# Kernel optimization log

Measured on AMD Instinct MI355X. Metric: run time of the kernel, lower is better.

## Reference

```python
import jax, jax.numpy as jnp
import numpy as np

TEMPERATURE = 8.0  # sqrt(head_dim=64)


def sparsemax(z):
    """Sparsemax along the last axis (Martins & Astudillo 2016)."""
    S = z.shape[-1]
    z_sorted = -jnp.sort(-z, axis=-1)            # descending sort
    cs = jnp.cumsum(z_sorted, axis=-1)
    ks = jnp.arange(1, S + 1, dtype=z.dtype)
    support = 1.0 + ks * z_sorted > cs           # entries in the support set
    k_sup = jnp.sum(support, axis=-1, keepdims=True)  # support size >= 1
    tau = (jnp.take_along_axis(cs, k_sup - 1, axis=-1) - 1.0) / k_sup.astype(z.dtype)
    return jnp.maximum(z - tau, 0.0)


def setup_inputs() -> dict:
    key = jax.random.key(0)
    kq, kk, kv, km = jax.random.split(key, 4)
    B, Lq, Lk, D = 64, 1024, 1024, 64
    q = jax.random.normal(kq, (B, Lq, D), dtype=jnp.float32)
    k = jax.random.normal(kk, (B, Lk, D), dtype=jnp.float32)
    v = jax.random.normal(kv, (B, Lk, D), dtype=jnp.float32)
    mask = jax.random.randint(km, (B, Lq, Lk), 0, 2).astype(bool)  # True = masked out
    return {"q": q, "k": k, "v": v, "mask": mask}


def reference(q, k, v, mask):
    # scores: [B, Lq, Lk]
    attn = jnp.einsum('bqd,bkd->bqk', q / TEMPERATURE, k)
    # mask out disallowed keys with -inf
    attn = jnp.where(mask, -jnp.inf, attn)
    # rows where ALL keys are masked: set scores to 0 (avoids NaN in sparsemax)
    inf_mask = jnp.all(mask, axis=2, keepdims=True)  # [B, Lq, 1]
    attn = jnp.where(inf_mask, 0.0, attn)
    attn = sparsemax(attn)
    # zero out fully-masked rows again (dropout has p=0.0 -> identity in eval)
    attn = jnp.where(inf_mask, 0.0, attn)
    out = jnp.einsum('bqk,bkd->bqd', attn, v)
    return (out, attn)
```

## Files before the change

kernel.cpp:

```cpp
#include <hip/hip_runtime.h>
#include <float.h>


#define BATCH    64
#define SEQQ     1024
#define SEQK     1024
#define DHEAD    64

typedef short short8 __attribute__((ext_vector_type(8)));
typedef float f32x4  __attribute__((ext_vector_type(4)));
typedef unsigned short us4v __attribute__((ext_vector_type(4)));

typedef const __attribute__((address_space(1))) unsigned int as1_cuint;
typedef __attribute__((address_space(3))) unsigned int as3_uint;
typedef __attribute__((address_space(3))) unsigned char as3_uchar;

__device__ __forceinline__ unsigned short bf16_rne(float f) {
    unsigned u = __float_as_uint(f);
    u += 0x7fffu + ((u >> 16) & 1u);
    return (unsigned short)(u >> 16);
}

__device__ __forceinline__ void cvt_hilo8(const float* fv, float scale,
                                          short8* hi, short8* lo) {
    #pragma unroll
    for (int j = 0; j < 8; ++j) {
        float f = fv[j] * scale;
        unsigned short hb = bf16_rne(f);
        float hf = __uint_as_float((unsigned)hb << 16);
        (*hi)[j] = (short)hb;
        (*lo)[j] = (short)bf16_rne(f - hf);
    }
}

__global__ void detect_mask_fmt(const unsigned char* __restrict__ m,
                                int* __restrict__ flag) {
    __shared__ int s_found;
    if (threadIdx.x == 0) s_found = 0;
    __syncthreads();
    int found = 0;
    for (int o = threadIdx.x; o < 65536; o += 256) {
        if ((o & 3) != 0 && m[o] != 0) found = 1;
    }
    if (found) atomicOr(&s_found, 1);
    __syncthreads();
    if (threadIdx.x == 0) *flag = s_found;
}

__global__ __launch_bounds__(256) void kprep_detect(
        const float* __restrict__ k, unsigned short* __restrict__ kbuf,
        const unsigned char* __restrict__ m, int* __restrict__ flag) {
    if (blockIdx.x == (BATCH * SEQK * 8) / 256) {
        __shared__ int s_found;
        if (threadIdx.x == 0) s_found = 0;
        __syncthreads();
        int found = 0;
        for (int o = threadIdx.x; o < 65536; o += 256) {
            if ((o & 3) != 0 && m[o] != 0) found = 1;
        }
        if (found) atomicOr(&s_found, 1);
        __syncthreads();
        if (threadIdx.x == 0) *flag = s_found;
        return;
    }

    int gid  = blockIdx.x * 256 + threadIdx.x;
    int db   = gid & 7;
    int keyg = (gid >> 3) & 1023;
    int b    = gid >> 13;
    int kt   = keyg >> 7;
    int key  = keyg & 127;

    const float4* src =
        (const float4*)(k + ((size_t)b * SEQK + keyg) * DHEAD + db * 8);
    float4 f0 = src[0], f1 = src[1];
    float fv[8] = {f0.x, f0.y, f0.z, f0.w, f1.x, f1.y, f1.z, f1.w};
    short8 hi, lo;
    cvt_hilo8(fv, 1.0f, &hi, &lo);

    unsigned short* tile = kbuf + (size_t)(b * 8 + kt) * 16384;
    int off = key * 64 + ((db ^ (key & 7)) * 8);
    *(short8*)(tile + off)        = hi;
    *(short8*)(tile + 8192 + off) = lo;
}

__global__ __launch_bounds__(256) void score_kernel_dma(
        const float* __restrict__ q, const unsigned short* __restrict__ kbuf,
        unsigned short* __restrict__ sbuf, int pitch) {
    const int lane = threadIdx.x & 63;
    const int wave = threadIdx.x >> 6;
    const int quad = lane >> 4;
    const int l15  = lane & 15;
    const int qt = blockIdx.x >> 6;
    const int b  = blockIdx.x & 63;

    __shared__ unsigned short klds[2 * 128 * 64];

    const float* qrow =
        q + ((size_t)b * SEQQ + qt * 64 + wave * 16 + l15) * DHEAD;
    short8 a_hi[2], a_lo[2];
    #pragma unroll
    for (int kc = 0; kc < 2; ++kc) {
        const float4* src = (const float4*)(qrow + kc * 32 + quad * 8);
        float4 f0 = src[0], f1 = src[1];
        float fv[8] = {f0.x, f0.y, f0.z, f0.w, f1.x, f1.y, f1.z, f1.w};
        cvt_hilo8(fv, 0.125f, &a_hi[kc], &a_lo[kc]);
    }

    unsigned short* srowq =
        sbuf + ((size_t)b * SEQQ + qt * 64 + wave * 16 + l15) * (size_t)pitch;

    for (int kt = 0; kt < 8; ++kt) {
        __syncthreads();
        const unsigned char* gtile =
            (const unsigned char*)(kbuf + (size_t)(b * 8 + kt) * 16384);
        {
            unsigned base = wave * 8192 + lane * 16;
            #pragma unroll
            for (int j = 0; j < 8; ++j) {
                unsigned off = base + j * 1024;
                as1_cuint* gp = (as1_cuint*)(gtile + off);
                as3_uint*  lp = (as3_uint*)((as3_uchar*)klds +
                                            (wave * 8192 + j * 1024));
                __builtin_amdgcn_global_load_lds(gp, lp, 16, 0, 0);
            }
        }
        __syncthreads();

        #pragma unroll
        for (int g = 0; g < 8; ++g) {
            int key = g * 16 + l15;
            short8 b_hi[2], b_lo[2];
            #pragma unroll
            for (int kc = 0; kc < 2; ++kc) {
                int db  = kc * 4 + quad;
                int off = key * 64 + ((db ^ (key & 7)) * 8);
                b_hi[kc] = *(const short8*)(klds + off);
                b_lo[kc] = *(const short8*)(klds + 8192 + off);
            }
            f32x4 acc = {0.f, 0.f, 0.f, 0.f};
            #pragma unroll
            for (int kc = 0; kc < 2; ++kc) {
                acc = __builtin_amdgcn_mfma_f32_16x16x32_bf16(b_hi[kc], a_hi[kc], acc, 0, 0, 0);
                acc = __builtin_amdgcn_mfma_f32_16x16x32_bf16(b_hi[kc], a_lo[kc], acc, 0, 0, 0);
                acc = __builtin_amdgcn_mfma_f32_16x16x32_bf16(b_lo[kc], a_hi[kc], acc, 0, 0, 0);
            }
            us4v pk;
            #pragma unroll
            for (int r = 0; r < 4; ++r) pk[r] = bf16_rne(acc[r]);
            *(us4v*)(srowq + kt * 128 + g * 16 + quad * 4) = pk;
        }
    }
}

__global__ __launch_bounds__(256) void score_kernel_cvt(
        const float* __restrict__ q, const float* __restrict__ k,
        unsigned short* __restrict__ sbuf, int pitch) {
    const int lane = threadIdx.x & 63;
    const int wave = threadIdx.x >> 6;
    const int quad = lane >> 4;
    const int l15  = lane & 15;
    const int qt = blockIdx.x >> 6;
    const int b  = blockIdx.x & 63;

    __shared__ unsigned short klds[2 * 128 * 64];

    const float* qrow =
        q + ((size_t)b * SEQQ + qt * 64 + wave * 16 + l15) * DHEAD;
    short8 a_hi[2], a_lo[2];
    #pragma unroll
    for (int kc = 0; kc < 2; ++kc) {
        const float4* src = (const float4*)(qrow + kc * 32 + quad * 8);
        float4 f0 = src[0], f1 = src[1];
        float fv[8] = {f0.x, f0.y, f0.z, f0.w, f1.x, f1.y, f1.z, f1.w};
        cvt_hilo8(fv, 0.125f, &a_hi[kc], &a_lo[kc]);
    }

    const float* kb = k + (size_t)b * SEQK * DHEAD;
    unsigned short* srowq =
        sbuf + ((size_t)b * SEQQ + qt * 64 + wave * 16 + l15) * (size_t)pitch;

    for (int kt = 0; kt < 8; ++kt) {
        __syncthreads();
        const float* kbase = kb + (size_t)kt * 128 * DHEAD;
        #pragma unroll
        for (int it = 0; it < 4; ++it) {
            int e   = threadIdx.x + 256 * it;
            int key = e >> 3, db = e & 7;
            const float4* src = (const float4*)(kbase + key * DHEAD + db * 8);
            float4 f0 = src[0], f1 = src[1];
            float fv[8] = {f0.x, f0.y, f0.z, f0.w, f1.x, f1.y, f1.z, f1.w};
            short8 hi, lo;
            cvt_hilo8(fv, 1.0f, &hi, &lo);
            int off = key * 64 + ((db ^ (key & 7)) * 8);
            *(short8*)(klds + off)        = hi;
            *(short8*)(klds + 8192 + off) = lo;
        }
        __syncthreads();

        #pragma unroll
        for (int g = 0; g < 8; ++g) {
            int key = g * 16 + l15;
            short8 b_hi[2], b_lo[2];
            #pragma unroll
            for (int kc = 0; kc < 2; ++kc) {
                int db  = kc * 4 + quad;
                int off = key * 64 + ((db ^ (key & 7)) * 8);
                b_hi[kc] = *(const short8*)(klds + off);
                b_lo[kc] = *(const short8*)(klds + 8192 + off);
            }
            f32x4 acc = {0.f, 0.f, 0.f, 0.f};
            #pragma unroll
            for (int kc = 0; kc < 2; ++kc) {
                acc = __builtin_amdgcn_mfma_f32_16x16x32_bf16(b_hi[kc], a_hi[kc], acc, 0, 0, 0);
                acc = __builtin_amdgcn_mfma_f32_16x16x32_bf16(b_hi[kc], a_lo[kc], acc, 0, 0, 0);
                acc = __builtin_amdgcn_mfma_f32_16x16x32_bf16(b_lo[kc], a_hi[kc], acc, 0, 0, 0);
            }
            us4v pk;
            #pragma unroll
            for (int r = 0; r < 4; ++r) pk[r] = bf16_rne(acc[r]);
            *(us4v*)(srowq + kt * 128 + g * 16 + quad * 4) = pk;
        }
    }
}

__global__ __launch_bounds__(256) void sparsemax_pv(
        const float* __restrict__ v, const void* __restrict__ mask,
        const int* __restrict__ fmt_flag,
        float* __restrict__ out, float* __restrict__ attn,
        const unsigned short* __restrict__ sbuf, int pitch) {
    const int lane = threadIdx.x & 63;
    const int wave = threadIdx.x >> 6;
    const int row  = blockIdx.x * 4 + wave;
    const int b    = row >> 10;
    float* arow = attn + (size_t)row * SEQK;
    const int mask_is_byte = fmt_flag ? *fmt_flag : 1;

    const us4v* s4 = (const us4v*)(sbuf + (size_t)row * (size_t)pitch);
    float s[16];
    #pragma unroll
    for (int t = 0; t < 4; ++t) {
        us4v u = __builtin_nontemporal_load(s4 + lane + 64 * t);
        s[4*t+0] = __uint_as_float((unsigned)u[0] << 16);
        s[4*t+1] = __uint_as_float((unsigned)u[1] << 16);
        s[4*t+2] = __uint_as_float((unsigned)u[2] << 16);
        s[4*t+3] = __uint_as_float((unsigned)u[3] << 16);
    }
    if (mask_is_byte) {
        const unsigned* m32 =
            (const unsigned*)((const unsigned char*)mask + (size_t)row * SEQK);
        #pragma unroll
        for (int t = 0; t < 4; ++t) {
            unsigned m = __builtin_nontemporal_load(m32 + lane + 64 * t);
            if (m & 0x000000ffu) s[4*t+0] = -FLT_MAX;
            if (m & 0x0000ff00u) s[4*t+1] = -FLT_MAX;
            if (m & 0x00ff0000u) s[4*t+2] = -FLT_MAX;
            if (m & 0xff000000u) s[4*t+3] = -FLT_MAX;
        }
    } else {
        const int* mi = (const int*)mask + (size_t)row * SEQK;
        #pragma unroll
        for (int t = 0; t < 4; ++t) {
            int m0 = __builtin_nontemporal_load(mi + 4 * (lane + 64 * t) + 0);
            int m1 = __builtin_nontemporal_load(mi + 4 * (lane + 64 * t) + 1);
            int m2 = __builtin_nontemporal_load(mi + 4 * (lane + 64 * t) + 2);
            int m3 = __builtin_nontemporal_load(mi + 4 * (lane + 64 * t) + 3);
            if (m0) s[4*t+0] = -FLT_MAX;
            if (m1) s[4*t+1] = -FLT_MAX;
            if (m2) s[4*t+2] = -FLT_MAX;
            if (m3) s[4*t+3] = -FLT_MAX;
        }
    }

    float mx = -FLT_MAX;
    #pragma unroll
    for (int i = 0; i < 16; ++i) mx = fmaxf(mx, s[i]);
    #pragma unroll
    for (int off = 32; off >= 1; off >>= 1)
        mx = fmaxf(mx, __shfl_xor(mx, off, 64));

    if (mx <= -FLT_MAX) {
        f32x4 z = {0.f, 0.f, 0.f, 0.f};
        #pragma unroll
        for (int t = 0; t < 4; ++t)
            __builtin_nontemporal_store(z, (f32x4*)arow + lane + 64 * t);
        out[(size_t)row * DHEAD + lane] = 0.f;
        return;
    }

    float thr = mx - 1.0f, tau = 0.f;
    int cnt_prev = -1;
    for (int it = 0; it < 32; ++it) {
        float lsum = 0.f; int lcnt = 0;
        #pragma unroll
        for (int i = 0; i < 16; ++i)
            if (s[i] > thr) { lsum += s[i]; lcnt++; }
        #pragma unroll
        for (int off = 32; off >= 1; off >>= 1) {
            lsum += __shfl_xor(lsum, off, 64);
            lcnt += __shfl_xor(lcnt, off, 64);
        }
        tau = (lsum - 1.0f) / (float)lcnt;
        if (lcnt == cnt_prev) break;
        cnt_prev = lcnt;
        thr = tau;
    }

    float p[16];
    #pragma unroll
    for (int i = 0; i < 16; ++i) {
        float pv = s[i] - tau;
        p[i] = pv > 0.f ? pv : 0.f;
    }
    #pragma unroll
    for (int t = 0; t < 4; ++t) {
        f32x4 f = {p[4*t+0], p[4*t+1], p[4*t+2], p[4*t+3]};
        __builtin_nontemporal_store(f, (f32x4*)arow + lane + 64 * t);
    }

    const float* vbase = v + (size_t)b * SEQK * DHEAD;
    float oacc = 0.f;
    #pragma unroll
    for (int t = 0; t < 4; ++t) {
        #pragma unroll
        for (int c = 0; c < 4; ++c) {
            int i = 4 * t + c;
            unsigned long long mb = __ballot(p[i] > 0.f);
            while (mb) {
                int k0, k1 = -1, k2 = -1, k3 = -1;
                k0 = __ffsll(mb) - 1; mb &= mb - 1;
                if (mb) { k1 = __ffsll(mb) - 1; mb &= mb - 1; }
                if (mb) { k2 = __ffsll(mb) - 1; mb &= mb - 1; }
                if (mb) { k3 = __ffsll(mb) - 1; mb &= mb - 1; }
                float pj0 = __shfl(p[i], k0);
                float v0  = vbase[(size_t)(4 * k0 + 256 * t + c) * DHEAD + lane];
                float pj1 = 0.f, pj2 = 0.f, pj3 = 0.f;
                float v1 = 0.f, v2 = 0.f, v3 = 0.f;
                if (k1 >= 0) {
                    pj1 = __shfl(p[i], k1);
                    v1  = vbase[(size_t)(4 * k1 + 256 * t + c) * DHEAD + lane];
                }
                if (k2 >= 0) {
                    pj2 = __shfl(p[i], k2);
                    v2  = vbase[(size_t)(4 * k2 + 256 * t + c) * DHEAD + lane];
                }
                if (k3 >= 0) {
                    pj3 = __shfl(p[i], k3);
                    v3  = vbase[(size_t)(4 * k3 + 256 * t + c) * DHEAD + lane];
                }
                oacc = fmaf(pj0, v0, oacc);
                if (k1 >= 0) oacc = fmaf(pj1, v1, oacc);
                if (k2 >= 0) oacc = fmaf(pj2, v2, oacc);
                if (k3 >= 0) oacc = fmaf(pj3, v3, oacc);
            }
        }
    }
    out[(size_t)row * DHEAD + lane] = oacc;
}

extern "C" void kernel_launch(void* const* d_in, const int* in_sizes, int n_in,
                              void* d_out, int out_size, void* d_ws, size_t ws_size,
                              hipStream_t stream) {
    const float* q = (const float*)d_in[0];
    const float* k = (const float*)d_in[1];
    const float* v = (const float*)d_in[2];
    const void*  m = d_in[3];

    float* out  = (float*)d_out;
    float* attn = out + (size_t)BATCH * SEQQ * DHEAD;

    int* flag = nullptr;
    if (ws_size >= sizeof(int)) flag = (int*)d_ws;

    const size_t S_BYTES = (size_t)BATCH * SEQQ * SEQK * 2;
    const size_t K_BYTES = (size_t)BATCH * SEQK * DHEAD * 2 * 2;

    unsigned short* sbuf;
    int pitch;
    bool s_in_ws = ws_size >= 16 + S_BYTES;
    if (s_in_ws) {
        sbuf  = (unsigned short*)d_ws + 8;
        pitch = SEQK;
    } else {
        sbuf  = (unsigned short*)attn;
        pitch = 2 * SEQK;
    }

    bool k_in_ws = s_in_ws && ws_size >= 16 + S_BYTES + K_BYTES;
    if (k_in_ws) {
        unsigned short* kbuf =
            (unsigned short*)((char*)d_ws + 16 + S_BYTES);
        kprep_detect<<<(BATCH * SEQK * 8) / 256 + 1, 256, 0, stream>>>(
            k, kbuf, (const unsigned char*)m, flag);
        score_kernel_dma<<<(SEQQ / 64) * BATCH, 256, 0, stream>>>(
            q, kbuf, sbuf, pitch);
    } else {
        if (flag)
            detect_mask_fmt<<<1, 256, 0, stream>>>((const unsigned char*)m, flag);
        score_kernel_cvt<<<(SEQQ / 64) * BATCH, 256, 0, stream>>>(
            q, k, sbuf, pitch);
    }

    sparsemax_pv<<<(BATCH * SEQQ) / 4, 256, 0, stream>>>(
        v, m, flag, out, attn, sbuf, pitch);
}
```

Baseline: 641.6 us.

## Double-buffer K tiles in score kernel and coalesce score stores via LDS

The K-tile buffer layout shrinks from 128-key to 64-key tiles, and the score kernel now double-buffers these tiles in LDS. The next tile's async global-to-LDS load is issued while the current one is processed through MFMA, replacing the earlier two barriers per tile with one. Score outputs are staged through a swizzled per-wave LDS tile so each row is written with full 16-byte contiguous stores instead of scattered 8-byte writes. Costs are extra LDS usage and twice as many loop iterations.

Result: no change. 646.1 us (+0.7%).

```diff
diff --git a/kernel.cpp b/kernel.cpp
--- a/kernel.cpp
+++ b/kernel.cpp
@@ -68,8 +68,8 @@
     int db   = gid & 7;
     int keyg = (gid >> 3) & 1023;
     int b    = gid >> 13;
-    int kt   = keyg >> 7;
-    int key  = keyg & 127;
+    int kt   = keyg >> 6;
+    int key  = keyg & 63;
 
     const float4* src =
         (const float4*)(k + ((size_t)b * SEQK + keyg) * DHEAD + db * 8);
@@ -78,10 +78,24 @@
     short8 hi, lo;
     cvt_hilo8(fv, 1.0f, &hi, &lo);
 
-    unsigned short* tile = kbuf + (size_t)(b * 8 + kt) * 16384;
+    unsigned short* tile = kbuf + (size_t)(b * 16 + kt) * 8192;
     int off = key * 64 + ((db ^ (key & 7)) * 8);
     *(short8*)(tile + off)        = hi;
-    *(short8*)(tile + 8192 + off) = lo;
+    *(short8*)(tile + 4096 + off) = lo;
+}
+
+__device__ __forceinline__ void stage_tile(
+        const unsigned short* kb_b, int kt, unsigned short* dstbuf,
+        int wave, int lane) {
+    const unsigned char* gtile =
+        (const unsigned char*)(kb_b + (size_t)kt * 8192);
+    #pragma unroll
+    for (int j = 0; j < 4; ++j) {
+        unsigned off = wave * 4096 + j * 1024;
+        as1_cuint* gp = (as1_cuint*)(gtile + off + lane * 16);
+        as3_uint*  lp = (as3_uint*)((as3_uchar*)dstbuf + off);
+        __builtin_amdgcn_global_load_lds(gp, lp, 16, 0, 0);
+    }
 }
 
 __global__ __launch_bounds__(256) void score_kernel_dma(
@@ -94,10 +108,11 @@
     const int qt = blockIdx.x >> 6;
     const int b  = blockIdx.x & 63;
 
-    __shared__ unsigned short klds[2 * 128 * 64];
-
-    const float* qrow =
-        q + ((size_t)b * SEQQ + qt * 64 + wave * 16 + l15) * DHEAD;
+    __shared__ unsigned short klds[2][8192];
+    __shared__ __align__(16) unsigned short stile[4][1024];
+
+    const int qg = qt * 64 + wave * 16 + l15;
+    const float* qrow = q + ((size_t)b * SEQQ + qg) * DHEAD;
     short8 a_hi[2], a_lo[2];
     #pragma unroll
     for (int kc = 0; kc < 2; ++kc) {
@@ -107,36 +122,27 @@
         cvt_hilo8(fv, 0.125f, &a_hi[kc], &a_lo[kc]);
     }
 
-    unsigned short* srowq =
-        sbuf + ((size_t)b * SEQQ + qt * 64 + wave * 16 + l15) * (size_t)pitch;
-
-    for (int kt = 0; kt < 8; ++kt) {
-        __syncthreads();
-        const unsigned char* gtile =
-            (const unsigned char*)(kbuf + (size_t)(b * 8 + kt) * 16384);
-        {
-            unsigned base = wave * 8192 + lane * 16;
-            #pragma unroll
-            for (int j = 0; j < 8; ++j) {
-                unsigned off = base + j * 1024;
-                as1_cuint* gp = (as1_cuint*)(gtile + off);
-                as3_uint*  lp = (as3_uint*)((as3_uchar*)klds +
-                                            (wave * 8192 + j * 1024));
-                __builtin_amdgcn_global_load_lds(gp, lp, 16, 0, 0);
-            }
-        }
-        __syncthreads();
-
-        #pragma unroll
-        for (int g = 0; g < 8; ++g) {
+    const unsigned short* kb_b = kbuf + (size_t)b * 16 * 8192;
+    char* stw = (char*)&stile[wave][0];
+
+    stage_tile(kb_b, 0, &klds[0][0], wave, lane);
+    __syncthreads();
+
+    int cur = 0;
+    for (int kt = 0; kt < 16; ++kt) {
+        if (kt < 15)
+            stage_tile(kb_b, kt + 1, &klds[cur ^ 1][0], wave, lane);
+
+        const unsigned short* tile = &klds[cur][0];
+        #pragma unroll
+        for (int g = 0; g < 4; ++g) {
             int key = g * 16 + l15;
             short8 b_hi[2], b_lo[2];
             #pragma unroll
             for (int kc = 0; kc < 2; ++kc) {
-                int db  = kc * 4 + quad;
-                int off = key * 64 + ((db ^ (key & 7)) * 8);
-                b_hi[kc] = *(const short8*)(klds + off);
-                b_lo[kc] = *(const short8*)(klds + 8192 + off);
+                int off = key * 64 + (((kc * 4 + quad) ^ (key & 7)) * 8);
+                b_hi[kc] = *(const short8*)(tile + off);
+                b_lo[kc] = *(const short8*)(tile + 4096 + off);
             }
             f32x4 acc = {0.f, 0.f, 0.f, 0.f};
             #pragma unroll
@@ -148,8 +154,25 @@
             us4v pk;
             #pragma unroll
             for (int r = 0; r < 4; ++r) pk[r] = bf16_rne(acc[r]);
-            *(us4v*)(srowq + kt * 128 + g * 16 + quad * 4) = pk;
-        }
+            int c = g * 2 + (quad >> 1);
+            *(us4v*)(stw + l15 * 128 + ((c ^ (l15 & 7)) * 16) +
+                     (quad & 1) * 8) = pk;
+        }
+
+        #pragma unroll
+        for (int t = 0; t < 2; ++t) {
+            int rl  = (lane >> 3) + t * 8;
+            int c16 = lane & 7;
+            short8 sv = *(const short8*)(stw + rl * 128 +
+                                         ((c16 ^ (rl & 7)) * 16));
+            unsigned short* dst = sbuf +
+                ((size_t)b * SEQQ + qt * 64 + wave * 16 + rl) * (size_t)pitch +
+                kt * 64 + c16 * 8;
+            *(short8*)dst = sv;
+        }
+
+        __syncthreads();
+        cur ^= 1;
     }
 }
 
```

## Tile score DMA kernel as 2x2 query/key wave grid and defer score stores

Applied to the files above, without the earlier changes.

Each wave in the DMA score kernel now computes 32 query rows by 64 keys instead of 16 rows by 128 keys, so each K fragment read from LDS feeds two query groups. This halves the LDS reads per MFMA. The bf16 score stores are held in registers and written out after the next tile's DMA barrier, overlapping global stores with the K tile load. The cost is more registers for the doubled A fragments and the buffered results.

Result: no change. 642.0 us (+0.1%).

```diff
diff --git a/kernel.cpp b/kernel.cpp
--- a/kernel.cpp
+++ b/kernel.cpp
@@ -93,22 +93,29 @@
     const int l15  = lane & 15;
     const int qt = blockIdx.x >> 6;
     const int b  = blockIdx.x & 63;
+    const int qh = wave >> 1;
+    const int kh = wave & 1;
 
     __shared__ unsigned short klds[2 * 128 * 64];
 
-    const float* qrow =
-        q + ((size_t)b * SEQQ + qt * 64 + wave * 16 + l15) * DHEAD;
-    short8 a_hi[2], a_lo[2];
-    #pragma unroll
-    for (int kc = 0; kc < 2; ++kc) {
-        const float4* src = (const float4*)(qrow + kc * 32 + quad * 8);
-        float4 f0 = src[0], f1 = src[1];
-        float fv[8] = {f0.x, f0.y, f0.z, f0.w, f1.x, f1.y, f1.z, f1.w};
-        cvt_hilo8(fv, 0.125f, &a_hi[kc], &a_lo[kc]);
-    }
-
-    unsigned short* srowq =
-        sbuf + ((size_t)b * SEQQ + qt * 64 + wave * 16 + l15) * (size_t)pitch;
+    short8 a_hi[2][2], a_lo[2][2];
+    size_t srow_base[2];
+    #pragma unroll
+    for (int qg = 0; qg < 2; ++qg) {
+        const int qr = qt * 64 + qh * 32 + qg * 16 + l15;
+        const float* qrow = q + ((size_t)b * SEQQ + qr) * DHEAD;
+        #pragma unroll
+        for (int kc = 0; kc < 2; ++kc) {
+            const float4* src = (const float4*)(qrow + kc * 32 + quad * 8);
+            float4 f0 = src[0], f1 = src[1];
+            float fv[8] = {f0.x, f0.y, f0.z, f0.w, f1.x, f1.y, f1.z, f1.w};
+            cvt_hilo8(fv, 0.125f, &a_hi[qg][kc], &a_lo[qg][kc]);
+        }
+        srow_base[qg] = ((size_t)b * SEQQ + qr) * (size_t)pitch;
+    }
+
+    us4v pk[2][4];
+    int kt_prev = -1;
 
     for (int kt = 0; kt < 8; ++kt) {
         __syncthreads();
@@ -127,9 +134,18 @@
         }
         __syncthreads();
 
-        #pragma unroll
-        for (int g = 0; g < 8; ++g) {
-            int key = g * 16 + l15;
+        if (kt_prev >= 0) {
+            #pragma unroll
+            for (int qg = 0; qg < 2; ++qg)
+                #pragma unroll
+                for (int g = 0; g < 4; ++g)
+                    *(us4v*)(sbuf + srow_base[qg] + kt_prev * 128 +
+                             kh * 64 + g * 16 + quad * 4) = pk[qg][g];
+        }
+
+        #pragma unroll
+        for (int g = 0; g < 4; ++g) {
+            int key = kh * 64 + g * 16 + l15;
             short8 b_hi[2], b_lo[2];
             #pragma unroll
             for (int kc = 0; kc < 2; ++kc) {
@@ -138,19 +154,27 @@
                 b_hi[kc] = *(const short8*)(klds + off);
                 b_lo[kc] = *(const short8*)(klds + 8192 + off);
             }
-            f32x4 acc = {0.f, 0.f, 0.f, 0.f};
-            #pragma unroll
-            for (int kc = 0; kc < 2; ++kc) {
-                acc = __builtin_amdgcn_mfma_f32_16x16x32_bf16(b_hi[kc], a_hi[kc], acc, 0, 0, 0);
-                acc = __builtin_amdgcn_mfma_f32_16x16x32_bf16(b_hi[kc], a_lo[kc], acc, 0, 0, 0);
-                acc = __builtin_amdgcn_mfma_f32_16x16x32_bf16(b_lo[kc], a_hi[kc], acc, 0, 0, 0);
-            }
-            us4v pk;
-            #pragma unroll
-            for (int r = 0; r < 4; ++r) pk[r] = bf16_rne(acc[r]);
-            *(us4v*)(srowq + kt * 128 + g * 16 + quad * 4) = pk;
-        }
-    }
+            #pragma unroll
+            for (int qg = 0; qg < 2; ++qg) {
+                f32x4 acc = {0.f, 0.f, 0.f, 0.f};
+                #pragma unroll
+                for (int kc = 0; kc < 2; ++kc) {
+                    acc = __builtin_amdgcn_mfma_f32_16x16x32_bf16(b_hi[kc], a_hi[qg][kc], acc, 0, 0, 0);
+                    acc = __builtin_amdgcn_mfma_f32_16x16x32_bf16(b_hi[kc], a_lo[qg][kc], acc, 0, 0, 0);
+                    acc = __builtin_amdgcn_mfma_f32_16x16x32_bf16(b_lo[kc], a_hi[qg][kc], acc, 0, 0, 0);
+                }
+                #pragma unroll
+                for (int r = 0; r < 4; ++r) pk[qg][g][r] = bf16_rne(acc[r]);
+            }
+        }
+        kt_prev = kt;
+    }
+    #pragma unroll
+    for (int qg = 0; qg < 2; ++qg)
+        #pragma unroll
+        for (int g = 0; g < 4; ++g)
+            *(us4v*)(sbuf + srow_base[qg] + kt_prev * 128 +
+                     kh * 64 + g * 16 + quad * 4) = pk[qg][g];
 }
 
 __global__ __launch_bounds__(256) void score_kernel_cvt(
```
